# Performance work log

Measured on AMD Instinct MI355X. Metric: run time of the kernel, lower is better.

The kernel has to match this reference:

```python
import jax, jax.numpy as jnp
import numpy as np

B, L, D, N_HEADS = 8, 512, 1024, 16
D_HEAD = D // N_HEADS


def _mha_fuzzy(x_q, x_k, x_v, Wq, bq, Wk, bk, Wv, bv, Wo, bo):
    """Multi-head fuzzy attention, product t-norm score function."""
    b, lq, d_model = x_q.shape
    lk = x_k.shape[1]

    def proj(x, W, bias, l):
        # [b, l, D] -> [b, h, l, d_head]
        return (x @ W + bias).reshape(b, l, N_HEADS, D_HEAD).transpose(0, 2, 1, 3)

    Q = proj(x_q, Wq, bq, lq)
    K = proj(x_k, Wk, bk, lk)
    V = proj(x_v, Wv, bv, lk)
    # fuzzy memberships in [0,1]
    mu_q = jax.nn.sigmoid(Q)
    mu_k = jax.nn.sigmoid(K)
    # product t-norm aggregated over feature dim (mean), then softmax normalize
    scores = jnp.einsum('bhid,bhjd->bhij', mu_q, mu_k) / D_HEAD  # [b,h,lq,lk]
    attn = jax.nn.softmax(scores, axis=-1)
    out = jnp.einsum('bhij,bhjd->bhid', attn, V)
    out = out.transpose(0, 2, 1, 3).reshape(b, lq, d_model)
    return out @ Wo + bo, attn.mean(axis=1)  # avg over heads


def setup_inputs() -> dict:
    key = jax.random.key(0)
    ks = jax.random.split(key, 16)
    s = 1.0 / np.sqrt(D)
    inp = {
        'text_features': jax.random.normal(ks[0], (B, L, D), jnp.float32),
        'image_features': jax.random.normal(ks[1], (B, L, D), jnp.float32),
        'Wq': jax.random.normal(ks[2], (D, D), jnp.float32) * s,
        'bq': jnp.zeros((D,), jnp.float32),
        'Wk': jax.random.normal(ks[3], (D, D), jnp.float32) * s,
        'bk': jnp.zeros((D,), jnp.float32),
        'Wv': jax.random.normal(ks[4], (D, D), jnp.float32) * s,
        'bv': jnp.zeros((D,), jnp.float32),
        'Wo': jax.random.normal(ks[5], (D, D), jnp.float32) * s,
        'bo': jnp.zeros((D,), jnp.float32),
        'W1': jax.random.normal(ks[6], (3 * D, D), jnp.float32) * (1.0 / np.sqrt(3 * D)),
        'b1': jnp.zeros((D,), jnp.float32),
        'W2': jax.random.normal(ks[7], (D, D), jnp.float32) * s,
        'b2': jnp.zeros((D,), jnp.float32),
    }
    return inp


def reference(text_features, image_features, Wq, bq, Wk, bk, Wv, bv, Wo, bo, W1, b1, W2, b2):
    # shared fuzzy attention module applied in both cross-modal directions
    text_cross, avg_attn = _mha_fuzzy(text_features, image_features, image_features,
                                      Wq, bq, Wk, bk, Wv, bv, Wo, bo)
    image_cross, _ = _mha_fuzzy(image_features, text_features, text_features,
                                Wq, bq, Wk, bk, Wv, bv, Wo, bo)
    combined = jnp.concatenate([text_features, image_features, text_cross], axis=-1)
    hidden = jax.nn.relu(combined @ W1 + b1)
    compositional_output = hidden @ W2 + b2
    return text_cross, image_cross, compositional_output, avg_attn
```

## Files before the change

kernel.cpp:

```cpp
#include <hip/hip_runtime.h>

#define NB 8
#define SL 512
#define DM 1024
#define NH 16
#define DH 64

using bfrag = __attribute__((ext_vector_type(8))) short;
using facc  = __attribute__((ext_vector_type(4))) float;

__device__ __forceinline__ float bf2f(ushort u) {
    return __uint_as_float(((unsigned)u) << 16);
}
__device__ __forceinline__ ushort f2bf(float f) {
    unsigned x = __float_as_uint(f);
    return (ushort)((x + 0x7FFFu + ((x >> 16) & 1u)) >> 16);
}
__device__ __forceinline__ unsigned pack2(float a, float b) {
    return (unsigned)f2bf(a) | ((unsigned)f2bf(b) << 16);
}
__device__ __forceinline__ void gload16(const ushort* g, ushort* l) {
    __builtin_amdgcn_global_load_lds(
        (const __attribute__((address_space(1))) unsigned*)g,
        (__attribute__((address_space(3))) unsigned*)l, 16, 0, 0);
}

__device__ __forceinline__ void tconv_body(const float* __restrict__ W,
                                           ushort* __restrict__ WT,
                                           const int R, const int C,
                                           const int c0, const int r0) {
    __shared__ ushort T[64][68];
    const int tid = threadIdx.x;
    #pragma unroll
    for (int rr = 0; rr < 4; ++rr) {
        const int r = (tid >> 4) + rr * 16;
        const int c4 = (tid & 15) * 4;
        const float4 f = *(const float4*)(W + (size_t)(r0 + r) * C + c0 + c4);
        T[c4+0][r] = f2bf(f.x); T[c4+1][r] = f2bf(f.y);
        T[c4+2][r] = f2bf(f.z); T[c4+3][r] = f2bf(f.w);
    }
    __syncthreads();
    #pragma unroll
    for (int rr = 0; rr < 4; ++rr) {
        const int c = (tid >> 4) + rr * 16;
        const int r4 = (tid & 15) * 4;
        *(ushort4*)(WT + (size_t)(c0 + c) * R + r0 + r4) =
            make_ushort4(T[c][r4+0], T[c][r4+1], T[c][r4+2], T[c][r4+3]);
    }
}

__global__ __launch_bounds__(256)
void prep_k(const float* __restrict__ text, const float* __restrict__ image,
            const float* __restrict__ Wq, const float* __restrict__ Wk,
            const float* __restrict__ Wv, const float* __restrict__ Wo,
            ushort* __restrict__ xbf, ushort* __restrict__ Wt,
            ushort* __restrict__ WoT)
{
    const int bid = blockIdx.x;
    const size_t SZc = (size_t)NB * SL * DM;
    if (bid < 8192) {
        const int half = bid >> 12;
        const float* s = half ? image : text;
        ushort* d = xbf + (size_t)half * SZc;
        const size_t i = ((size_t)(bid & 4095) * 256 + threadIdx.x) * 4;
        const float4 f = *(const float4*)(s + i);
        *(ushort4*)(d + i) =
            make_ushort4(f2bf(f.x), f2bf(f.y), f2bf(f.z), f2bf(f.w));
    } else {
        const int t = bid - 8192;
        const int wsel = t >> 8, tt = t & 255;
        const float* W = (wsel == 0) ? Wq : (wsel == 1) ? Wk
                       : (wsel == 2) ? Wv : Wo;
        ushort* WT = (wsel < 3) ? Wt + (size_t)wsel * DM * DM : WoT;
        tconv_body(W, WT, DM, DM, (tt & 15) * 64, (tt >> 4) * 64);
    }
}

__global__ __launch_bounds__(256)
void tconvW12_k(const float* __restrict__ W1, const float* __restrict__ W2,
                ushort* __restrict__ W1T, ushort* __restrict__ W2T)
{
    const int bid = blockIdx.x;
    if (bid < 768)
        tconv_body(W1, W1T, 3 * DM, DM, (bid & 15) * 64, (bid >> 4) * 64);
    else {
        const int t = bid - 768;
        tconv_body(W2, W2T, DM, DM, (t & 15) * 64, (t >> 4) * 64);
    }
}

template<int ACT, int OMODE>
__global__ __launch_bounds__(256, 2)
void mfma_gemm(const ushort* __restrict__ A0, const ushort* __restrict__ A1,
               const float* __restrict__ A2f, const ushort* __restrict__ A2b,
               const int KA1, const int KA2, const int Ktot,
               const int lda, const int ldaf,
               const ushort* __restrict__ AM1, const int Msplit,
               const ushort* __restrict__ BT, const int ldb,
               const float* __restrict__ bias, const float* __restrict__ biasK,
               const float* __restrict__ biasV,
               float* __restrict__ outf, ushort* __restrict__ outb,
               ushort* __restrict__ outbK, ushort* __restrict__ outbVT,
               const int clustN)
{
    __shared__ ushort sh[32768];
    const int tid  = threadIdx.x;
    const int w    = tid >> 6;
    const int lane = tid & 63;
    const int ln   = lane & 15, qd = lane >> 4;
    const int wm = (w & 1) * 64, wn = (w >> 1) * 64;

    const int NTg = gridDim.x, MTg = gridDim.y;
    const int L   = blockIdx.x + NTg * blockIdx.y;
    const int xcd = L & 7, sIdx = L >> 3;
    int mt, nt;
    if (clustN) { const int np = NTg >> 3; nt = xcd * np + sIdx % np; mt = sIdx / np; }
    else        { mt = xcd * (MTg >> 3) + sIdx / NTg; nt = sIdx - (sIdx / NTg) * NTg; }
    const int m0 = mt * 128, n0 = nt * 128;

    const ushort* A0u = A0; const ushort* A1u = A1; int m0A = m0;
    if (Msplit && m0 >= Msplit) { A0u = AM1; A1u = AM1; m0A = m0 - Msplit; }

    const int arow = (lane >> 3);
    const int kc8s = ((lane & 7) ^ arow) * 8;

    facc acc[4][4];
    #pragma unroll
    for (int i = 0; i < 4; ++i)
        #pragma unroll
        for (int j = 0; j < 4; ++j)
            acc[i][j] = (facc){0.f, 0.f, 0.f, 0.f};

    auto stage = [&](int k0, ushort* buf) {
        ushort* Asb = buf;
        ushort* Bsb = buf + 8192;
        #pragma unroll
        for (int t = 0; t < 4; ++t) {
            const int c = w * 4 + t;
            gload16(BT + (size_t)(n0 + c * 8 + arow) * ldb + k0 + kc8s,
                    &Bsb[c * 512]);
        }
        if (k0 < KA2) {
            const ushort* Ab; int ko;
            if (k0 < KA1) { Ab = A0u; ko = k0; }
            else          { Ab = A1u; ko = k0 - KA1; }
            #pragma unroll
            for (int t = 0; t < 4; ++t) {
                const int c = w * 4 + t;
                gload16(Ab + (size_t)(m0A + c * 8 + arow) * lda + ko + kc8s,
                        &Asb[c * 512]);
            }
        } else if (A2b) {
            const int ko = k0 - KA2;
            #pragma unroll
            for (int t = 0; t < 4; ++t) {
                const int c = w * 4 + t;
                gload16(A2b + (size_t)(m0A + c * 8 + arow) * ldaf + ko + kc8s,
                        &Asb[c * 512]);
            }
        } else {
            const int ko = k0 - KA2;
            #pragma unroll
            for (int t = 0; t < 4; ++t) {
                const int c = w * 4 + t;
                const float* src = A2f + (size_t)(m0A + c * 8 + arow) * ldaf + ko + kc8s;
                const float4 f0 = *(const float4*)src;
                const float4 f1 = *(const float4*)(src + 4);
                uint4 p;
                p.x = pack2(f0.x, f0.y); p.y = pack2(f0.z, f0.w);
                p.z = pack2(f1.x, f1.y); p.w = pack2(f1.z, f1.w);
                *(uint4*)&Asb[c * 512 + lane * 8] = p;
            }
        }
    };

    stage(0, sh);
    for (int k0 = 0; k0 < Ktot; k0 += 64) {
        ushort* cur = sh + ((k0 >> 6) & 1) * 16384;
        ushort* nxt = sh + (((k0 >> 6) & 1) ^ 1) * 16384;
        __syncthreads();
        if (k0 + 64 < Ktot) stage(k0 + 64, nxt);
        ushort* Asb = cur;
        ushort* Bsb = cur + 8192;
        #pragma unroll
        for (int ks = 0; ks < 2; ++ks) {
            const int ch = (ks * 4 + qd) ^ (ln & 7);
            bfrag af[4], bfv[4];
            #pragma unroll
            for (int i = 0; i < 4; ++i)
                af[i] = *(const bfrag*)&Asb[(wm + i*16 + ln) * 64 + ch * 8];
            #pragma unroll
            for (int j = 0; j < 4; ++j)
                bfv[j] = *(const bfrag*)&Bsb[(wn + j*16 + ln) * 64 + ch * 8];
            #pragma unroll
            for (int i = 0; i < 4; ++i)
                #pragma unroll
                for (int j = 0; j < 4; ++j)
                    acc[i][j] = __builtin_amdgcn_mfma_f32_16x16x32_bf16(
                        af[i], bfv[j], acc[i][j], 0, 0, 0);
        }
    }

    if (OMODE == 4) {
        const int seg   = n0 >> 10;
        const int nloc0 = n0 & 1023;
        const float* bs = (seg == 0) ? bias : (seg == 1) ? biasK : biasV;
        if (seg < 2) {
            ushort* ob = (seg == 0) ? outb : outbK;
            #pragma unroll
            for (int j = 0; j < 4; ++j) {
                const int nl = nloc0 + wn + j * 16 + ln;
                const float bn = bs[nl];
                #pragma unroll
                for (int i = 0; i < 4; ++i) {
                    const int mb = m0 + wm + i * 16 + qd * 4;
                    #pragma unroll
                    for (int r = 0; r < 4; ++r) {
                        const float v = 1.f / (1.f + __expf(-(acc[i][j][r] + bn)));
                        const int m = mb + r;
                        const int g = m >> 9, l = m & 511;
                        ob[(((size_t)(g * NH + (nl >> 6))) * SL + l) * DH + (nl & 63)]
                            = f2bf(v);
                    }
                }
            }
        } else {
            __syncthreads();
            #pragma unroll
            for (int j = 0; j < 4; ++j) {
                const int n_l = wn + j * 16 + ln;
                const float bn = bs[nloc0 + n_l];
                #pragma unroll
                for (int i = 0; i < 4; ++i) {
                    #pragma unroll
                    for (int r = 0; r < 4; ++r) {
                        const int m_l = wm + i * 16 + qd * 4 + r;
                        const int c = (m_l >> 3) ^ (n_l & 7);
                        sh[n_l * 128 + c * 8 + (m_l & 7)] = f2bf(acc[i][j][r] + bn);
                    }
                }
            }
            __syncthreads();
            const int n_l = tid >> 1, half = tid & 1;
            const int nl = nloc0 + n_l;
            const int g = m0 >> 9, l0 = m0 & 511;
            ushort* dst = outbVT +
                (((size_t)(g * NH + (nl >> 6))) * DH + (nl & 63)) * SL + l0;
            #pragma unroll
            for (int u = 0; u < 8; ++u) {
                const int c = half * 8 + u;
                const int cs = c ^ (n_l & 7);
                *(uint4*)(dst + c * 8) = *(const uint4*)&sh[n_l * 128 + cs * 8];
            }
        }
        return;
    }

    #pragma unroll
    for (int j = 0; j < 4; ++j) {
        const int n = n0 + wn + j * 16 + ln;
        const float bn = bias[n];
        #pragma unroll
        for (int i = 0; i < 4; ++i) {
            const int mb = m0 + wm + i * 16 + qd * 4;
            #pragma unroll
            for (int r = 0; r < 4; ++r) {
                float v = acc[i][j][r] + bn;
                if (ACT == 1)      v = 1.f / (1.f + __expf(-v));
                else if (ACT == 2) v = v > 0.f ? v : 0.f;
                const int m = mb + r;
                if (OMODE == 0)      outf[(size_t)m * DM + n] = v;
                else if (OMODE == 2) outb[(size_t)m * DM + n] = f2bf(v);
                else {
                    outf[(size_t)m * DM + n] = v;
                    if (m < Msplit) outb[(size_t)m * DM + n] = f2bf(v);
                }
            }
        }
    }
}

__global__ __launch_bounds__(256, 2)
void attn2m_k(const ushort* __restrict__ Qm, const ushort* __restrict__ Km,
              const ushort* __restrict__ VTm, ushort* __restrict__ AO0,
              ushort* __restrict__ AO1, float* __restrict__ RS0,
              float* __restrict__ RS1)
{
    __shared__ ushort Ks[128 * 64];
    __shared__ ushort VTs[64 * 128];
    __shared__ ushort Es[128 * 128];
    const int tid  = threadIdx.x;
    const int w    = tid >> 6;
    const int lane = tid & 63;
    const int ln   = lane & 15, qd = lane >> 4;
    const int wm  = (w & 1) * 64;
    const int wns = (w >> 1) * 64;
    const int wnd = (w >> 1) * 32;
    const int qt = blockIdx.x, h = blockIdx.y;
    const int zz = blockIdx.z;
    const int dir = zz >> 3, b = zz & 7;
    const size_t HALFc = (size_t)NB * SL * DM;
    const ushort* Qall = Qm  + (dir ? HALFc : 0);
    const ushort* Kall = Km  + (dir ? 0 : HALFc);
    const ushort* Vall = VTm + (dir ? 0 : HALFc);
    ushort* AOp = dir ? AO1 : AO0;
    float*  RSp = dir ? RS1 : RS0;

    const size_t ho = ((size_t)(b * NH + h)) * SL * DH;
    const ushort* Qg  = Qall + ho + (size_t)qt * 128 * DH;
    const ushort* Kg  = Kall + ho;
    const ushort* VTg = Vall + ho;

    bfrag qf[4][2];
    #pragma unroll
    for (int i = 0; i < 4; ++i)
        #pragma unroll
        for (int ks = 0; ks < 2; ++ks)
            qf[i][ks] = *(const bfrag*)(Qg + (size_t)(wm + i*16 + ln) * DH + ks*32 + qd*8);

    facc oacc[4][2];
    #pragma unroll
    for (int i = 0; i < 4; ++i)
        #pragma unroll
        for (int j = 0; j < 2; ++j)
            oacc[i][j] = (facc){0.f, 0.f, 0.f, 0.f};
    float rp[4][4];
    #pragma unroll
    for (int i = 0; i < 4; ++i)
        #pragma unroll
        for (int r = 0; r < 4; ++r)
            rp[i][r] = 0.f;

    const int arow = lane >> 3;
    const int kc8s = ((lane & 7) ^ arow) * 8;
    const int vrow = lane >> 4;

    for (int kc = 0; kc < 4; ++kc) {
        __syncthreads();
        #pragma unroll
        for (int t = 0; t < 4; ++t) {
            const int c = w * 4 + t;
            const int vc8s = ((lane & 15) ^ ((c * 4 + vrow) & 7)) * 8;
            gload16(Kg + (size_t)(kc*128 + c*8 + arow) * DH + kc8s, &Ks[c * 512]);
            gload16(VTg + (size_t)(c*4 + vrow) * SL + kc*128 + vc8s, &VTs[c * 512]);
        }
        __syncthreads();

        facc sacc[4][4];
        #pragma unroll
        for (int i = 0; i < 4; ++i)
            #pragma unroll
            for (int j = 0; j < 4; ++j)
                sacc[i][j] = (facc){0.f, 0.f, 0.f, 0.f};
        #pragma unroll
        for (int ks = 0; ks < 2; ++ks) {
            const int ch = (ks * 4 + qd) ^ (ln & 7);
            bfrag kf[4];
            #pragma unroll
            for (int j = 0; j < 4; ++j)
                kf[j] = *(const bfrag*)&Ks[(wns + j*16 + ln) * 64 + ch * 8];
            #pragma unroll
            for (int i = 0; i < 4; ++i)
                #pragma unroll
                for (int j = 0; j < 4; ++j)
                    sacc[i][j] = __builtin_amdgcn_mfma_f32_16x16x32_bf16(
                        qf[i][ks], kf[j], sacc[i][j], 0, 0, 0);
        }

        #pragma unroll
        for (int i = 0; i < 4; ++i) {
            #pragma unroll
            for (int r = 0; r < 4; ++r) {
                const int q = wm + i*16 + qd*4 + r;
                float p = 0.f;
                #pragma unroll
                for (int j = 0; j < 4; ++j) {
                    const float e = __expf(sacc[i][j][r] * 0.015625f);
                    const int key = wns + j*16 + ln;
                    const int c = (key >> 3) ^ (q & 7);
                    Es[q * 128 + c * 8 + (key & 7)] = f2bf(e);
                    p += e;
                }
                rp[i][r] += p;
            }
        }
        __syncthreads();

        #pragma unroll
        for (int ks2 = 0; ks2 < 4; ++ks2) {
            const int vch = (ks2 * 4 + qd) ^ (ln & 7);
            bfrag ea[4], vb[2];
            #pragma unroll
            for (int i = 0; i < 4; ++i) {
                const int q = wm + i*16 + ln;
                const int cs = (ks2*4 + qd) ^ (q & 7);
                ea[i] = *(const bfrag*)&Es[q * 128 + cs * 8];
            }
            #pragma unroll
            for (int j = 0; j < 2; ++j)
                vb[j] = *(const bfrag*)&VTs[(wnd + j*16 + ln) * 128 + vch * 8];
            #pragma unroll
            for (int i = 0; i < 4; ++i)
                #pragma unroll
                for (int j = 0; j < 2; ++j)
                    oacc[i][j] = __builtin_amdgcn_mfma_f32_16x16x32_bf16(
                        ea[i], vb[j], oacc[i][j], 0, 0, 0);
        }
    }

    #pragma unroll
    for (int i = 0; i < 4; ++i) {
        #pragma unroll
        for (int r = 0; r < 4; ++r) {
            float p = rp[i][r];
            p += __shfl_xor(p, 1, 16);
            p += __shfl_xor(p, 2, 16);
            p += __shfl_xor(p, 4, 16);
            p += __shfl_xor(p, 8, 16);
            rp[i][r] = p;
        }
    }

    __syncthreads();
    float* rsls = (float*)Ks;
    if (ln == 0) {
        #pragma unroll
        for (int i = 0; i < 4; ++i)
            #pragma unroll
            for (int r = 0; r < 4; ++r)
                rsls[(w >> 1) * 128 + wm + i*16 + qd*4 + r] = rp[i][r];
    }
    __syncthreads();
    if (tid < 128) {
        const float t = rsls[tid] + rsls[128 + tid];
        RSp[(size_t)(b * NH + h) * SL + qt * 128 + tid] = t;
        rsls[tid] = t;
    }
    __syncthreads();

    #pragma unroll
    for (int i = 0; i < 4; ++i) {
        #pragma unroll
        for (int r = 0; r < 4; ++r) {
            const int q = wm + i*16 + qd*4 + r;
            const float inv = 1.f / rsls[q];
            const size_t rowo = ((size_t)(b*SL + qt*128 + q)) * DM + h*DH;
            #pragma unroll
            for (int j = 0; j < 2; ++j)
                AOp[rowo + wnd + j*16 + ln] = f2bf(oacc[i][j][r] * inv);
        }
    }
}

__global__ __launch_bounds__(256, 2)
void avg3_k(const ushort* __restrict__ Qm, const ushort* __restrict__ Km,
            const float* __restrict__ RS, float* __restrict__ avga)
{
    __shared__ ushort Qs[64 * 64];
    __shared__ ushort Kt[64 * 64];
    __shared__ float rss[64];
    const int tid  = threadIdx.x;
    const int w    = tid >> 6;
    const int lane = tid & 63;
    const int ln   = lane & 15, qd = lane >> 4;
    const int wq = (w & 1) * 32, wk = (w >> 1) * 32;
    const int kt = blockIdx.x, qt = blockIdx.y, b = blockIdx.z;

    const int arow = lane >> 3;
    const int kc8s = ((lane & 7) ^ arow) * 8;

    float acc[2][2][4];
    #pragma unroll
    for (int i = 0; i < 2; ++i)
        #pragma unroll
        for (int j = 0; j < 2; ++j)
            #pragma unroll
            for (int r = 0; r < 4; ++r)
                acc[i][j][r] = 0.f;

    for (int h = 0; h < NH; ++h) {
        const size_t ho = ((size_t)(b * NH + h)) * SL * DH;
        __syncthreads();
        #pragma unroll
        for (int t = 0; t < 2; ++t) {
            const int c = w * 2 + t;
            gload16(Qm + ho + (size_t)(qt*64 + c*8 + arow) * DH + kc8s, &Qs[c * 512]);
            gload16(Km + ho + (size_t)(kt*64 + c*8 + arow) * DH + kc8s, &Kt[c * 512]);
        }
        if (tid < 64) rss[tid] = RS[(size_t)(b*NH + h)*SL + qt*64 + tid];
        __syncthreads();

        facc s[2][2];
        #pragma unroll
        for (int i = 0; i < 2; ++i)
            #pragma unroll
            for (int j = 0; j < 2; ++j)
                s[i][j] = (facc){0.f, 0.f, 0.f, 0.f};
        #pragma unroll
        for (int ks = 0; ks < 2; ++ks) {
            const int ch = (ks * 4 + qd) ^ (ln & 7);
            bfrag qa[2], kb[2];
            #pragma unroll
            for (int i = 0; i < 2; ++i)
                qa[i] = *(const bfrag*)&Qs[(wq + i*16 + ln) * 64 + ch * 8];
            #pragma unroll
            for (int j = 0; j < 2; ++j)
                kb[j] = *(const bfrag*)&Kt[(wk + j*16 + ln) * 64 + ch * 8];
            #pragma unroll
            for (int i = 0; i < 2; ++i)
                #pragma unroll
                for (int j = 0; j < 2; ++j)
                    s[i][j] = __builtin_amdgcn_mfma_f32_16x16x32_bf16(
                        qa[i], kb[j], s[i][j], 0, 0, 0);
        }
        #pragma unroll
        for (int i = 0; i < 2; ++i) {
            #pragma unroll
            for (int r = 0; r < 4; ++r) {
                const float ir = 0.0625f / rss[wq + i*16 + qd*4 + r];
                #pragma unroll
                for (int j = 0; j < 2; ++j)
                    acc[i][j][r] += __expf(s[i][j][r] * 0.015625f) * ir;
            }
        }
    }
    #pragma unroll
    for (int i = 0; i < 2; ++i) {
        #pragma unroll
        for (int r = 0; r < 4; ++r) {
            const int q = wq + i*16 + qd*4 + r;
            #pragma unroll
            for (int j = 0; j < 2; ++j)
                avga[((size_t)(b*SL + qt*64 + q)) * SL + kt*64 + wk + j*16 + ln]
                    = acc[i][j][r];
        }
    }
}

extern "C" void kernel_launch(void* const* d_in, const int* in_sizes, int n_in,
                              void* d_out, int out_size, void* d_ws, size_t ws_size,
                              hipStream_t stream)
{
    (void)in_sizes; (void)n_in; (void)out_size;
    const float* text  = (const float*)d_in[0];
    const float* image = (const float*)d_in[1];
    const float* Wq = (const float*)d_in[2];
    const float* bq = (const float*)d_in[3];
    const float* Wk = (const float*)d_in[4];
    const float* bk = (const float*)d_in[5];
    const float* Wv = (const float*)d_in[6];
    const float* bv = (const float*)d_in[7];
    const float* Wo = (const float*)d_in[8];
    const float* bo = (const float*)d_in[9];
    const float* W1 = (const float*)d_in[10];
    const float* b1 = (const float*)d_in[11];
    const float* W2 = (const float*)d_in[12];
    const float* b2 = (const float*)d_in[13];
    float* out = (float*)d_out;

    const size_t SZ   = (size_t)NB * SL * DM;
    const size_t HALF = SZ;

    ushort* xbf = (ushort*)d_ws;
    ushort* Qb  = xbf + 2*SZ;
    ushort* Kb  = Qb  + 2*SZ;
    ushort* VT  = Kb  + 2*SZ;
    ushort* AOt = VT  + 2*SZ;
    ushort* Wt  = AOt + SZ;
    float*  RS  = (float*)(Wt + 3*DM*DM);
    char*   wsEnd = (char*)(RS + NB*NH*SL);
    ushort* hidden = Qb;
    ushort* W2T    = AOt;

    float* text_cross = out;
    float* comp       = out + 2*SZ;
    float* avga       = out + 3*SZ;

    const size_t extBytes = (size_t)NB*NH*SL*4 + (size_t)DM*DM*2 + (size_t)SZ*2;
    const size_t fixBytes = (size_t)(wsEnd - (char*)d_ws);
    float* RS2; ushort* WoT; ushort* AOi;
    if (ws_size >= fixBytes + extBytes) {
        RS2 = (float*)wsEnd;
        WoT = (ushort*)(RS2 + NB*NH*SL);
        AOi = WoT + DM*DM;
    } else {
        WoT = (ushort*)comp;
        AOi = WoT + DM*DM;
        RS2 = (float*)Wt;
    }

    const dim3 blk(256);

    prep_k<<<9216, blk, 0, stream>>>(text, image, Wq, Wk, Wv, Wo, xbf, Wt, WoT);

    mfma_gemm<0,4><<<dim3(24,64), blk, 0, stream>>>(
        xbf, xbf, nullptr, nullptr, DM, DM, DM, DM, DM, nullptr, 0,
        Wt, DM, bq, bk, bv, nullptr, Qb, Kb, VT, 1);

    attn2m_k<<<dim3(SL/128, NH, 16), blk, 0, stream>>>(Qb, Kb, VT, AOt, AOi, RS, RS2);
    avg3_k<<<dim3(SL/64, SL/64, NB), blk, 0, stream>>>(Qb, Kb + HALF, RS, avga);

    mfma_gemm<0,5><<<dim3(8,64), blk, 0, stream>>>(
        AOt, AOt, nullptr, nullptr, DM, DM, DM, DM, DM, AOi, 4096,
        WoT, DM, bo, nullptr, nullptr, text_cross, Kb, nullptr, nullptr, 0);

    tconvW12_k<<<1024, blk, 0, stream>>>(W1, W2, Wt, W2T);

    mfma_gemm<2,2><<<dim3(8,32), blk, 0, stream>>>(
        xbf, xbf + SZ, nullptr, Kb, DM, 2*DM, 3*DM, DM, DM, nullptr, 0,
        Wt, 3*DM, b1, nullptr, nullptr, nullptr, hidden, nullptr, nullptr, 0);
    mfma_gemm<0,0><<<dim3(8,32), blk, 0, stream>>>(
        hidden, hidden, nullptr, nullptr, DM, DM, DM, DM, DM, nullptr, 0,
        W2T, DM, b2, nullptr, nullptr, comp, nullptr, nullptr, nullptr, 0);
}
```

Baseline: 375.3 us.

## Transpose score MFMA and remap attention grid for XCD-local K/V reuse

```diff
diff --git a/kernel.cpp b/kernel.cpp
--- a/kernel.cpp
+++ b/kernel.cpp
@@ -296,9 +296,15 @@
     const int wm  = (w & 1) * 64;
     const int wns = (w >> 1) * 64;
     const int wnd = (w >> 1) * 32;
-    const int qt = blockIdx.x, h = blockIdx.y;
-    const int zz = blockIdx.z;
+
+    const int L   = blockIdx.x;
+    const int xcd = L & 7, s = L >> 3;
+    const int qt  = s & 3;
+    const int pid = xcd * 32 + (s >> 2);
+    const int h   = pid & 15;
+    const int zz  = pid >> 4;
     const int dir = zz >> 3, b = zz & 7;
+
     const size_t HALFc = (size_t)NB * SL * DM;
     const ushort* Qall = Qm  + (dir ? HALFc : 0);
     const ushort* Kall = Km  + (dir ? 0 : HALFc);
@@ -324,12 +330,10 @@
         #pragma unroll
         for (int j = 0; j < 2; ++j)
             oacc[i][j] = (facc){0.f, 0.f, 0.f, 0.f};
-    float rp[4][4];
+    float rp[4];
     #pragma unroll
     for (int i = 0; i < 4; ++i)
-        #pragma unroll
-        for (int r = 0; r < 4; ++r)
-            rp[i][r] = 0.f;
+        rp[i] = 0.f;
 
     const int arow = lane >> 3;
     const int kc8s = ((lane & 7) ^ arow) * 8;
@@ -348,10 +352,10 @@
 
         facc sacc[4][4];
         #pragma unroll
-        for (int i = 0; i < 4; ++i)
-            #pragma unroll
-            for (int j = 0; j < 4; ++j)
-                sacc[i][j] = (facc){0.f, 0.f, 0.f, 0.f};
+        for (int j = 0; j < 4; ++j)
+            #pragma unroll
+            for (int i = 0; i < 4; ++i)
+                sacc[j][i] = (facc){0.f, 0.f, 0.f, 0.f};
         #pragma unroll
         for (int ks = 0; ks < 2; ++ks) {
             const int ch = (ks * 4 + qd) ^ (ln & 7);
@@ -360,29 +364,33 @@
             for (int j = 0; j < 4; ++j)
                 kf[j] = *(const bfrag*)&Ks[(wns + j*16 + ln) * 64 + ch * 8];
             #pragma unroll
-            for (int i = 0; i < 4; ++i)
+            for (int j = 0; j < 4; ++j)
                 #pragma unroll
-                for (int j = 0; j < 4; ++j)
-                    sacc[i][j] = __builtin_amdgcn_mfma_f32_16x16x32_bf16(
-                        qf[i][ks], kf[j], sacc[i][j], 0, 0, 0);
+                for (int i = 0; i < 4; ++i)
+                    sacc[j][i] = __builtin_amdgcn_mfma_f32_16x16x32_bf16(
+                        kf[j], qf[i][ks], sacc[j][i], 0, 0, 0);
         }
 
         #pragma unroll
         for (int i = 0; i < 4; ++i) {
-            #pragma unroll
-            for (int r = 0; r < 4; ++r) {
-                const int q = wm + i*16 + qd*4 + r;
-                float p = 0.f;
-                #pragma unroll
-                for (int j = 0; j < 4; ++j) {
-                    const float e = __expf(sacc[i][j][r] * 0.015625f);
-                    const int key = wns + j*16 + ln;
-                    const int c = (key >> 3) ^ (q & 7);
-                    Es[q * 128 + c * 8 + (key & 7)] = f2bf(e);
-                    p += e;
-                }
-                rp[i][r] += p;
-            }
+            const int q  = wm + i*16 + ln;
+            const int qs = q & 7;
+            float p = 0.f;
+            #pragma unroll
+            for (int j = 0; j < 4; ++j) {
+                const int key0 = wns + j*16 + qd*4;
+                const float e0 = __expf(sacc[j][i][0] * 0.015625f);
+                const float e1 = __expf(sacc[j][i][1] * 0.015625f);
+                const float e2 = __expf(sacc[j][i][2] * 0.015625f);
+                const float e3 = __expf(sacc[j][i][3] * 0.015625f);
+                const int c = ((key0 & 127) >> 3) ^ qs;
+                uint2 pk;
+                pk.x = pack2(e0, e1);
+                pk.y = pack2(e2, e3);
+                *(uint2*)&Es[q * 128 + c * 8 + (key0 & 7)] = pk;
+                p += (e0 + e1) + (e2 + e3);
+            }
+            rp[i] += p;
         }
         __syncthreads();
 
@@ -410,25 +418,18 @@
 
     #pragma unroll
     for (int i = 0; i < 4; ++i) {
-        #pragma unroll
-        for (int r = 0; r < 4; ++r) {
-            float p = rp[i][r];
-            p += __shfl_xor(p, 1, 16);
-            p += __shfl_xor(p, 2, 16);
-            p += __shfl_xor(p, 4, 16);
-            p += __shfl_xor(p, 8, 16);
-            rp[i][r] = p;
-        }
+        float p = rp[i];
+        p += __shfl_xor(p, 16);
+        p += __shfl_xor(p, 32);
+        rp[i] = p;
     }
 
     __syncthreads();
     float* rsls = (float*)Ks;
-    if (ln == 0) {
+    if (qd == 0) {
         #pragma unroll
         for (int i = 0; i < 4; ++i)
-            #pragma unroll
-            for (int r = 0; r < 4; ++r)
-                rsls[(w >> 1) * 128 + wm + i*16 + qd*4 + r] = rp[i][r];
+            rsls[(w >> 1) * 128 + wm + i*16 + ln] = rp[i];
     }
     __syncthreads();
     if (tid < 128) {
@@ -597,7 +598,7 @@
         xbf, xbf, nullptr, nullptr, DM, DM, DM, DM, DM, nullptr, 0,
         Wt, DM, bq, bk, bv, nullptr, Qb, Kb, VT, 1);
 
-    attn2m_k<<<dim3(SL/128, NH, 16), blk, 0, stream>>>(Qb, Kb, VT, AOt, AOi, RS, RS2);
+    attn2m_k<<<dim3(1024), blk, 0, stream>>>(Qb, Kb, VT, AOt, AOi, RS, RS2);
     avg3_k<<<dim3(SL/64, SL/64, NB), blk, 0, stream>>>(Qb, Kb + HALF, RS, avga);
 
     mfma_gemm<0,5><<<dim3(8,64), blk, 0, stream>>>(
```

After: 338.5 us. 9.8% less time.
